# Kernel tuning notes

Measured on AMD Instinct MI355X. Metric: run time of the kernel, lower is better.

Reference implementation:

```python
import jax, jax.numpy as jnp
import numpy as np

BS, NE, IN_DIM = 1024, 128, 512
EMBED, OUT_DIM = 512, 512
N_HEADS, N_AGENTS = 8, 32
HEAD_DIM = EMBED // N_HEADS


def setup_inputs() -> dict:
    key = jax.random.key(0)
    ks = jax.random.split(key, 6)
    entities = jax.random.normal(ks[0], (BS, NE, IN_DIM), dtype=jnp.float32)
    pre_mask = jax.random.bernoulli(ks[1], 0.3, (BS, N_AGENTS, NE))
    post_mask = jax.random.bernoulli(ks[2], 0.3, (BS, N_AGENTS))
    # parameters (torch Linear convention: W @ x, i.e. [out, in])
    W_in = jax.random.normal(ks[3], (3 * EMBED, IN_DIM), dtype=jnp.float32) / np.sqrt(IN_DIM)
    W_out = jax.random.normal(ks[4], (OUT_DIM, EMBED), dtype=jnp.float32) / np.sqrt(EMBED)
    b_out = jax.random.normal(ks[5], (OUT_DIM,), dtype=jnp.float32) * 0.01
    return {"entities": entities, "pre_mask": pre_mask, "post_mask": post_mask,
            "W_in": W_in, "W_out": W_out, "b_out": b_out}


def reference(entities, pre_mask, post_mask, W_in, W_out, b_out):
    bs, ne, _ = entities.shape
    qkv = entities @ W_in.T                      # [bs, ne, 3*embed]
    q, k, v = jnp.split(qkv, 3, axis=-1)
    q = q[:, :N_AGENTS]                          # [bs, na, embed]
    q = q.reshape(bs, N_AGENTS, N_HEADS, HEAD_DIM)
    k = k.reshape(bs, ne, N_HEADS, HEAD_DIM)
    v = v.reshape(bs, ne, N_HEADS, HEAD_DIM)
    scale = jnp.sqrt(jnp.float32(HEAD_DIM))
    logits = jnp.einsum('bahd,behd->bhae', q, k) / scale   # [bs, h, na, ne]
    masked = jnp.where(pre_mask[:, None], -jnp.inf, logits)
    w = jax.nn.softmax(masked, axis=-1)
    w = jnp.where(jnp.isnan(w), 0.0, w)          # fully-masked rows -> 0 (NaN cleanup)
    attn = jnp.einsum('bhae,behd->bahd', w, v).reshape(bs, N_AGENTS, EMBED)
    out = attn @ W_out.T + b_out                 # [bs, na, out_dim]
    out = jnp.where(post_mask[:, :, None], 0.0, out)
    return out
```

## Files before the change

### kernel.cpp

```cpp
#include <hip/hip_runtime.h>
#include <hip/hip_bf16.h>
#include <stdint.h>


#define NE_ 128
#define NA_ 32
#define NH_ 8
#define HD_ 64
#define IND_ 512
#define EMB_ 512

typedef __attribute__((ext_vector_type(8))) __bf16 bf16x8;
typedef __attribute__((ext_vector_type(4))) float f32x4;

static __device__ __forceinline__ unsigned short bfu(float x) {
  __hip_bfloat16 h = __float2bfloat16(x);
  union { __hip_bfloat16 h1; unsigned short u; } c; c.h1 = h; return c.u;
}
static __device__ __forceinline__ unsigned int pack2(float x, float y) {
  return (unsigned int)bfu(x) | ((unsigned int)bfu(y) << 16);
}
static __device__ __forceinline__ void gload16(const void* g, const void* l) {
  __builtin_amdgcn_global_load_lds(
      (const __attribute__((address_space(1))) unsigned int*)g,
      (__attribute__((address_space(3))) unsigned int*)l, 16, 0, 0);
}

__global__ __launch_bounds__(256)
void k0_convert(const float* __restrict__ win, const float* __restrict__ wout,
                unsigned short* __restrict__ wb) {
  int t = blockIdx.x * 256 + threadIdx.x;
  int i = t * 4;
  float4 v;
  if (i < 786432) v = *(const float4*)(win + i);
  else            v = *(const float4*)(wout + (i - 786432));
  uint2 pk; pk.x = pack2(v.x, v.y); pk.y = pack2(v.z, v.w);
  *(uint2*)(wb + i) = pk;
}

struct K1Lds {
  union {
    struct { unsigned short a[128 * 64]; unsigned short b[192 * 64]; } st;
    struct {
      union { float s[32 * 132]; unsigned short attn[32 * 72]; } x;
      unsigned short p[32 * 136];
    } sm;
  } u;
  unsigned short kk[128 * 72];
  unsigned short vT[64 * 136];
  unsigned short qq[32 * 72];
};

__global__ __launch_bounds__(256, 2)
void k1_fused(const float* __restrict__ ent, const int* __restrict__ pre,
              const unsigned short* __restrict__ wb, unsigned short* __restrict__ attn_out) {
  __shared__ K1Lds sh;
  const int tid = threadIdx.x;
  const int w = tid >> 6, l = tid & 63;
  const int n = blockIdx.x;
  const int xcd = n & 7, kid = n >> 3;
  const int b = xcd * 128 + (kid >> 3);
  const int h = kid & 7;

  const float* E = ent + (size_t)b * (NE_ * IND_);
  char* aB = (char*)sh.u.st.a;
  char* bB = (char*)sh.u.st.b;

  f32x4 acc[2][12];
#pragma unroll
  for (int i = 0; i < 2; ++i)
#pragma unroll
    for (int j = 0; j < 12; ++j) acc[i][j] = (f32x4){0.f, 0.f, 0.f, 0.f};

  const int trow = tid >> 4, tc4 = tid & 15;
  const int hi16 = (l >> 4) << 4;

  for (int kt = 0; kt < 8; ++kt) {
    __syncthreads();
#pragma unroll
    for (int i = 0; i < 8; ++i) {
      int row = trow + i * 16;
      const float4 v = *(const float4*)(E + row * 512 + kt * 64 + tc4 * 4);
      uint2 pk; pk.x = pack2(v.x, v.y); pk.y = pack2(v.z, v.w);
      int x = (row * 128 + tc4 * 8) ^ ((row & 7) << 4);
      *(uint2*)(aB + x) = pk;
    }
#pragma unroll
    for (int i = 0; i < 6; ++i) {
      int c = w * 6 + i;
      int x = c * 1024 + l * 16;
      int y = x ^ (((x >> 7) & 7) << 4);
      int idx = y >> 1;
      int r = idx >> 6, col = idx & 63;
      int wrow = ((r >> 6) << 9) + h * 64 + (r & 63);
      gload16(wb + (size_t)wrow * 512 + kt * 64 + col, bB + c * 1024);
    }
    __syncthreads();
#pragma unroll
    for (int ks = 0; ks < 2; ++ks) {
      bf16x8 af[2];
#pragma unroll
      for (int i = 0; i < 2; ++i) {
        int row = (w * 2 + i) * 16 + (l & 15);
        int off = (row * 128 + ks * 64 + hi16) ^ ((row & 7) << 4);
        af[i] = *(const bf16x8*)(aB + off);
      }
#pragma unroll
      for (int j = 0; j < 12; ++j) {
        int r = j * 16 + (l & 15);
        int off = (r * 128 + ks * 64 + hi16) ^ ((r & 7) << 4);
        bf16x8 bf = *(const bf16x8*)(bB + off);
        acc[0][j] = __builtin_amdgcn_mfma_f32_16x16x32_bf16(af[0], bf, acc[0][j], 0, 0, 0);
        acc[1][j] = __builtin_amdgcn_mfma_f32_16x16x32_bf16(af[1], bf, acc[1][j], 0, 0, 0);
      }
    }
  }

  {
    const int col16 = l & 15, rg = l >> 4;
#pragma unroll
    for (int i = 0; i < 2; ++i) {
      int mrow = (w * 2 + i) * 16 + rg * 4;
      if (w == 0) {
#pragma unroll
        for (int j = 0; j < 4; ++j) {
          int d = j * 16 + col16;
#pragma unroll
          for (int r = 0; r < 4; ++r) sh.qq[(mrow + r) * 72 + d] = bfu(acc[i][j][r] * 0.125f);
        }
      }
#pragma unroll
      for (int j = 4; j < 8; ++j) {
        int d = (j - 4) * 16 + col16;
#pragma unroll
        for (int r = 0; r < 4; ++r) sh.kk[(mrow + r) * 72 + d] = bfu(acc[i][j][r]);
      }
#pragma unroll
      for (int j = 8; j < 12; ++j) {
        int d = (j - 8) * 16 + col16;
        uint2 pk;
        pk.x = pack2(acc[i][j][0], acc[i][j][1]);
        pk.y = pack2(acc[i][j][2], acc[i][j][3]);
        *(uint2*)((char*)sh.vT + d * 272 + mrow * 2) = pk;
      }
    }
  }
  __syncthreads();

  {
    f32x4 sacc[2][2];
#pragma unroll
    for (int i = 0; i < 2; ++i)
#pragma unroll
      for (int j = 0; j < 2; ++j) sacc[i][j] = (f32x4){0.f, 0.f, 0.f, 0.f};
    char* qB = (char*)sh.qq;
    char* kB = (char*)sh.kk;
#pragma unroll
    for (int ks = 0; ks < 2; ++ks) {
      bf16x8 qf[2];
#pragma unroll
      for (int at = 0; at < 2; ++at) {
        int row = at * 16 + (l & 15);
        qf[at] = *(const bf16x8*)(qB + row * 144 + ks * 64 + hi16);
      }
#pragma unroll
      for (int je = 0; je < 2; ++je) {
        int e = (2 * w + je) * 16 + (l & 15);
        bf16x8 kf = *(const bf16x8*)(kB + e * 144 + ks * 64 + hi16);
        sacc[0][je] = __builtin_amdgcn_mfma_f32_16x16x32_bf16(qf[0], kf, sacc[0][je], 0, 0, 0);
        sacc[1][je] = __builtin_amdgcn_mfma_f32_16x16x32_bf16(qf[1], kf, sacc[1][je], 0, 0, 0);
      }
    }
    float* S = sh.u.sm.x.s;
#pragma unroll
    for (int at = 0; at < 2; ++at)
#pragma unroll
      for (int je = 0; je < 2; ++je) {
        int e = (2 * w + je) * 16 + (l & 15);
        int a0 = at * 16 + (l >> 4) * 4;
#pragma unroll
        for (int r = 0; r < 4; ++r) S[(a0 + r) * 132 + e] = sacc[at][je][r];
      }
  }
  __syncthreads();

  {
    int a = tid >> 3, ls = tid & 7;
    const int* pm = pre + ((size_t)b * NA_ + a) * NE_ + ls * 16;
    const float* srow = sh.u.sm.x.s + a * 132 + ls * 16;
    float sv[16]; int mk[16];
    float mx = -__builtin_inff();
#pragma unroll
    for (int c = 0; c < 4; ++c) {
      int4 m4 = *(const int4*)(pm + c * 4);
      float4 s4 = *(const float4*)(srow + c * 4);
      mk[c * 4 + 0] = m4.x; sv[c * 4 + 0] = s4.x;
      mk[c * 4 + 1] = m4.y; sv[c * 4 + 1] = s4.y;
      mk[c * 4 + 2] = m4.z; sv[c * 4 + 2] = s4.z;
      mk[c * 4 + 3] = m4.w; sv[c * 4 + 3] = s4.w;
    }
#pragma unroll
    for (int i = 0; i < 16; ++i)
      if (!mk[i]) mx = fmaxf(mx, sv[i]);
    mx = fmaxf(mx, __shfl_xor(mx, 1));
    mx = fmaxf(mx, __shfl_xor(mx, 2));
    mx = fmaxf(mx, __shfl_xor(mx, 4));
    const bool dead = (mx == -__builtin_inff());
    float pv[16]; float sum = 0.f;
#pragma unroll
    for (int i = 0; i < 16; ++i) {
      float p = (mk[i] || dead) ? 0.f : __expf(sv[i] - mx);
      pv[i] = p; sum += p;
    }
    sum += __shfl_xor(sum, 1);
    sum += __shfl_xor(sum, 2);
    sum += __shfl_xor(sum, 4);
    float inv = dead ? 0.f : (1.f / sum);
    unsigned short* P = sh.u.sm.p + a * 136 + ls * 16;
#pragma unroll
    for (int c = 0; c < 4; ++c) {
      uint2 pk;
      pk.x = pack2(pv[c * 4 + 0] * inv, pv[c * 4 + 1] * inv);
      pk.y = pack2(pv[c * 4 + 2] * inv, pv[c * 4 + 3] * inv);
      *(uint2*)(P + c * 4) = pk;
    }
  }
  __syncthreads();

  {
    char* pB = (char*)sh.u.sm.p;
    char* vB = (char*)sh.vT;
    int at = w >> 1, dt0 = (w & 1) * 2;
    f32x4 pacc[2] = {(f32x4){0.f, 0.f, 0.f, 0.f}, (f32x4){0.f, 0.f, 0.f, 0.f}};
#pragma unroll
    for (int ks = 0; ks < 4; ++ks) {
      int arow = at * 16 + (l & 15);
      bf16x8 pf = *(const bf16x8*)(pB + arow * 272 + ks * 64 + hi16);
#pragma unroll
      for (int jd = 0; jd < 2; ++jd) {
        int d = (dt0 + jd) * 16 + (l & 15);
        bf16x8 vf = *(const bf16x8*)(vB + d * 272 + ks * 64 + hi16);
        pacc[jd] = __builtin_amdgcn_mfma_f32_16x16x32_bf16(pf, vf, pacc[jd], 0, 0, 0);
      }
    }
    unsigned short* A = sh.u.sm.x.attn;
#pragma unroll
    for (int jd = 0; jd < 2; ++jd) {
      int d = (dt0 + jd) * 16 + (l & 15);
      int a0 = at * 16 + (l >> 4) * 4;
#pragma unroll
      for (int r = 0; r < 4; ++r) A[(a0 + r) * 72 + d] = bfu(pacc[jd][r]);
    }
  }
  __syncthreads();

  {
    int row = tid >> 3, c8 = (tid & 7) * 8;
    uint4 v = *(const uint4*)((const char*)sh.u.sm.x.attn + row * 144 + c8 * 2);
    *(uint4*)(attn_out + ((size_t)(b * NA_ + row) * EMB_ + h * HD_ + c8)) = v;
  }
}

__global__ __launch_bounds__(256, 2)
void k2_out(const unsigned short* __restrict__ attn, const unsigned short* __restrict__ wob,
            const float* __restrict__ bout, const int* __restrict__ post,
            float* __restrict__ out) {
  __shared__ struct { unsigned short a[128 * 64]; unsigned short b[128 * 64]; } sh;
  const int tid = threadIdx.x, w = tid >> 6, l = tid & 63;
  const int n = blockIdx.x;
  const int sw = (n & 7) * 128 + (n >> 3);
  const int mt = sw >> 2, ntb = sw & 3;
  char* aB = (char*)sh.a;
  char* bB = (char*)sh.b;
  const int hi16 = (l >> 4) << 4;

  f32x4 acc[2][8];
#pragma unroll
  for (int i = 0; i < 2; ++i)
#pragma unroll
    for (int j = 0; j < 8; ++j) acc[i][j] = (f32x4){0.f, 0.f, 0.f, 0.f};

  for (int kt = 0; kt < 8; ++kt) {
    __syncthreads();
#pragma unroll
    for (int i = 0; i < 4; ++i) {
      int c = w * 4 + i;
      int x = c * 1024 + l * 16;
      int y = x ^ (((x >> 7) & 7) << 4);
      int idx = y >> 1, r = idx >> 6, col = idx & 63;
      gload16(attn + (size_t)(mt * 128 + r) * 512 + kt * 64 + col, aB + c * 1024);
      gload16(wob + (size_t)(ntb * 128 + r) * 512 + kt * 64 + col, bB + c * 1024);
    }
    __syncthreads();
#pragma unroll
    for (int ks = 0; ks < 2; ++ks) {
      bf16x8 af[2];
#pragma unroll
      for (int i = 0; i < 2; ++i) {
        int row = (w * 2 + i) * 16 + (l & 15);
        af[i] = *(const bf16x8*)(aB + ((row * 128 + ks * 64 + hi16) ^ ((row & 7) << 4)));
      }
#pragma unroll
      for (int j = 0; j < 8; ++j) {
        int r = j * 16 + (l & 15);
        bf16x8 bf = *(const bf16x8*)(bB + ((r * 128 + ks * 64 + hi16) ^ ((r & 7) << 4)));
        acc[0][j] = __builtin_amdgcn_mfma_f32_16x16x32_bf16(af[0], bf, acc[0][j], 0, 0, 0);
        acc[1][j] = __builtin_amdgcn_mfma_f32_16x16x32_bf16(af[1], bf, acc[1][j], 0, 0, 0);
      }
    }
  }

  int pmv[2][4];
#pragma unroll
  for (int i = 0; i < 2; ++i) {
    int m0 = mt * 128 + w * 32 + i * 16 + (l >> 4) * 4;
#pragma unroll
    for (int r = 0; r < 4; ++r) pmv[i][r] = post[m0 + r];
  }
#pragma unroll
  for (int j = 0; j < 8; ++j) {
    int nn = ntb * 128 + j * 16 + (l & 15);
    float bo = bout[nn];
#pragma unroll
    for (int i = 0; i < 2; ++i) {
      int m0 = mt * 128 + w * 32 + i * 16 + (l >> 4) * 4;
#pragma unroll
      for (int r = 0; r < 4; ++r) {
        float v = pmv[i][r] ? 0.f : (acc[i][j][r] + bo);
        out[(size_t)(m0 + r) * 512 + nn] = v;
      }
    }
  }
}

extern "C" void kernel_launch(void* const* d_in, const int* in_sizes, int n_in,
                              void* d_out, int out_size, void* d_ws, size_t ws_size,
                              hipStream_t stream) {
  const float* ent  = (const float*)d_in[0];
  const int*   pre  = (const int*)d_in[1];
  const int*   post = (const int*)d_in[2];
  const float* win  = (const float*)d_in[3];
  const float* wout = (const float*)d_in[4];
  const float* bout = (const float*)d_in[5];
  float* out = (float*)d_out;

  unsigned short* wsb   = (unsigned short*)d_ws;
  unsigned short* winb  = wsb;
  unsigned short* woutb = wsb + 786432;
  unsigned short* attnb = wsb + 1048576;

  hipLaunchKernelGGL(k0_convert, dim3(1024), dim3(256), 0, stream, win, wout, wsb);
  hipLaunchKernelGGL(k1_fused, dim3(8192), dim3(256), 0, stream, ent, pre, winb, attnb);
  hipLaunchKernelGGL(k2_out, dim3(1024), dim3(256), 0, stream, attnb, woutb, bout, post, out);
}
```

Measured before the change: 695.8 us.

## Split Q projection into own kernel, process two heads per block

Adds a separate GEMM kernel that projects only the 32 agent rows to Q and writes it to workspace. The fused attention kernel now covers two heads per 512-thread block and computes only K/V with larger 4x4 MFMA warp tiles. The old code computed Q for all 128 entities and discarded most of it. Fewer blocks each reread the entity tile and convert it to bf16, which cuts redundant fp32 reads and conversions. The output GEMM also moves to 256-row tiles with 512 threads. The cost is an extra launch, a Q round trip through global memory, and more LDS per block, which may limit occupancy.

```diff
diff --git a/kernel.cpp b/kernel.cpp
--- a/kernel.cpp
+++ b/kernel.cpp
@@ -2,13 +2,6 @@
 #include <hip/hip_bf16.h>
 #include <stdint.h>
 
-
-#define NE_ 128
-#define NA_ 32
-#define NH_ 8
-#define HD_ 64
-#define IND_ 512
-#define EMB_ 512
 
 typedef __attribute__((ext_vector_type(8))) __bf16 bf16x8;
 typedef __attribute__((ext_vector_type(4))) float f32x4;
@@ -38,295 +31,370 @@
   *(uint2*)(wb + i) = pk;
 }
 
+__global__ __launch_bounds__(256, 3)
+void kq_qproj(const float* __restrict__ ent, const unsigned short* __restrict__ wb,
+              unsigned short* __restrict__ q_ws) {
+  __shared__ union {
+    struct { unsigned short a[128 * 64]; unsigned short b[128 * 64]; } st;
+    unsigned short rs[128 * 136];
+  } sh;
+  const int tid = threadIdx.x, w = tid >> 6, l = tid & 63;
+  const int n = blockIdx.x;
+  const int sw = (n & 7) * 128 + (n >> 3);
+  const int mt = sw >> 2, ntb = sw & 3;
+  char* aB = (char*)sh.st.a;
+  char* bB = (char*)sh.st.b;
+  const int hi16 = (l >> 4) << 4;
+  const int trow = tid >> 4, tc4 = tid & 15;
+
+  f32x4 acc[2][8];
+#pragma unroll
+  for (int i = 0; i < 2; ++i)
+#pragma unroll
+    for (int j = 0; j < 8; ++j) acc[i][j] = (f32x4){0.f, 0.f, 0.f, 0.f};
+
+  for (int kt = 0; kt < 8; ++kt) {
+    __syncthreads();
+#pragma unroll
+    for (int i = 0; i < 8; ++i) {
+      int row = trow + i * 16;
+      int gr = mt * 128 + row;
+      const float4 v = *(const float4*)(ent + (size_t)(gr >> 5) * 65536 + (gr & 31) * 512 + kt * 64 + tc4 * 4);
+      uint2 pk; pk.x = pack2(v.x, v.y); pk.y = pack2(v.z, v.w);
+      int x = (row * 128 + tc4 * 8) ^ ((row & 7) << 4);
+      *(uint2*)(aB + x) = pk;
+    }
+#pragma unroll
+    for (int i = 0; i < 4; ++i) {
+      int c = w * 4 + i;
+      int x = c * 1024 + l * 16;
+      int y = x ^ (((x >> 7) & 7) << 4);
+      int idx = y >> 1, r = idx >> 6, col = idx & 63;
+      gload16(wb + (size_t)(ntb * 128 + r) * 512 + kt * 64 + col, bB + c * 1024);
+    }
+    __syncthreads();
+#pragma unroll
+    for (int ks = 0; ks < 2; ++ks) {
+      bf16x8 af[2];
+#pragma unroll
+      for (int i = 0; i < 2; ++i) {
+        int row = (w * 2 + i) * 16 + (l & 15);
+        af[i] = *(const bf16x8*)(aB + ((row * 128 + ks * 64 + hi16) ^ ((row & 7) << 4)));
+      }
+#pragma unroll
+      for (int j = 0; j < 8; ++j) {
+        int r = j * 16 + (l & 15);
+        bf16x8 bf = *(const bf16x8*)(bB + ((r * 128 + ks * 64 + hi16) ^ ((r & 7) << 4)));
+        acc[0][j] = __builtin_amdgcn_mfma_f32_16x16x32_bf16(af[0], bf, acc[0][j], 0, 0, 0);
+        acc[1][j] = __builtin_amdgcn_mfma_f32_16x16x32_bf16(af[1], bf, acc[1][j], 0, 0, 0);
+      }
+    }
+  }
+  __syncthreads();
+#pragma unroll
+  for (int i = 0; i < 2; ++i) {
+    int row0 = w * 32 + i * 16 + (l >> 4) * 4;
+#pragma unroll
+    for (int j = 0; j < 8; ++j) {
+      int col = j * 16 + (l & 15);
+#pragma unroll
+      for (int r = 0; r < 4; ++r) sh.rs[(row0 + r) * 136 + col] = bfu(acc[i][j][r] * 0.125f);
+    }
+  }
+  __syncthreads();
+#pragma unroll
+  for (int it = 0; it < 8; ++it) {
+    int row = it * 16 + (tid >> 4), c8 = (tid & 15) * 8;
+    uint4 v = *(const uint4*)((const char*)sh.rs + row * 272 + c8 * 2);
+    int gr = mt * 128 + row;
+    int b = gr >> 5, a = gr & 31;
+    int c = ntb * 128 + c8;
+    int h = c >> 6, d = c & 63;
+    *(uint4*)(q_ws + (((size_t)b * 8 + h) * 32 + a) * 64 + d) = v;
+  }
+}
+
 struct K1Lds {
   union {
-    struct { unsigned short a[128 * 64]; unsigned short b[192 * 64]; } st;
+    struct { unsigned short a[128 * 64]; unsigned short b[256 * 64]; } st;
     struct {
-      union { float s[32 * 132]; unsigned short attn[32 * 72]; } x;
+      unsigned short kk[128 * 72];
+      unsigned short vT[64 * 136];
+      unsigned short qq[32 * 72];
+      float s[32 * 132];
       unsigned short p[32 * 136];
+      unsigned short at[32 * 72];
     } sm;
   } u;
-  unsigned short kk[128 * 72];
-  unsigned short vT[64 * 136];
-  unsigned short qq[32 * 72];
 };
 
-__global__ __launch_bounds__(256, 2)
+__global__ __launch_bounds__(512, 4)
 void k1_fused(const float* __restrict__ ent, const int* __restrict__ pre,
-              const unsigned short* __restrict__ wb, unsigned short* __restrict__ attn_out) {
+              const unsigned short* __restrict__ wb, const unsigned short* __restrict__ q_ws,
+              unsigned short* __restrict__ attn_out) {
   __shared__ K1Lds sh;
   const int tid = threadIdx.x;
   const int w = tid >> 6, l = tid & 63;
   const int n = blockIdx.x;
   const int xcd = n & 7, kid = n >> 3;
-  const int b = xcd * 128 + (kid >> 3);
-  const int h = kid & 7;
-
-  const float* E = ent + (size_t)b * (NE_ * IND_);
+  const int b = xcd * 128 + (kid >> 2);
+  const int h2 = kid & 3;
+
+  const float* E = ent + (size_t)b * (128 * 512);
   char* aB = (char*)sh.u.st.a;
   char* bB = (char*)sh.u.st.b;
-
-  f32x4 acc[2][12];
-#pragma unroll
-  for (int i = 0; i < 2; ++i)
-#pragma unroll
-    for (int j = 0; j < 12; ++j) acc[i][j] = (f32x4){0.f, 0.f, 0.f, 0.f};
-
-  const int trow = tid >> 4, tc4 = tid & 15;
   const int hi16 = (l >> 4) << 4;
+  const int wr = w >> 2;
+  const int wq = w & 3;
+
+  f32x4 acc[4][4];
+#pragma unroll
+  for (int i = 0; i < 4; ++i)
+#pragma unroll
+    for (int j = 0; j < 4; ++j) acc[i][j] = (f32x4){0.f, 0.f, 0.f, 0.f};
 
   for (int kt = 0; kt < 8; ++kt) {
     __syncthreads();
-#pragma unroll
-    for (int i = 0; i < 8; ++i) {
-      int row = trow + i * 16;
-      const float4 v = *(const float4*)(E + row * 512 + kt * 64 + tc4 * 4);
-      uint2 pk; pk.x = pack2(v.x, v.y); pk.y = pack2(v.z, v.w);
-      int x = (row * 128 + tc4 * 8) ^ ((row & 7) << 4);
-      *(uint2*)(aB + x) = pk;
-    }
-#pragma unroll
-    for (int i = 0; i < 6; ++i) {
-      int c = w * 6 + i;
-      int x = c * 1024 + l * 16;
-      int y = x ^ (((x >> 7) & 7) << 4);
-      int idx = y >> 1;
-      int r = idx >> 6, col = idx & 63;
-      int wrow = ((r >> 6) << 9) + h * 64 + (r & 63);
-      gload16(wb + (size_t)wrow * 512 + kt * 64 + col, bB + c * 1024);
-    }
-    __syncthreads();
-#pragma unroll
-    for (int ks = 0; ks < 2; ++ks) {
-      bf16x8 af[2];
-#pragma unroll
-      for (int i = 0; i < 2; ++i) {
-        int row = (w * 2 + i) * 16 + (l & 15);
-        int off = (row * 128 + ks * 64 + hi16) ^ ((row & 7) << 4);
-        af[i] = *(const bf16x8*)(aB + off);
-      }
-#pragma unroll
-      for (int j = 0; j < 12; ++j) {
-        int r = j * 16 + (l & 15);
-        int off = (r * 128 + ks * 64 + hi16) ^ ((r & 7) << 4);
-        bf16x8 bf = *(const bf16x8*)(bB + off);
-        acc[0][j] = __builtin_amdgcn_mfma_f32_16x16x32_bf16(af[0], bf, acc[0][j], 0, 0, 0);
-        acc[1][j] = __builtin_amdgcn_mfma_f32_16x16x32_bf16(af[1], bf, acc[1][j], 0, 0, 0);
-      }
-    }
-  }
-
-  {
-    const int col16 = l & 15, rg = l >> 4;
-#pragma unroll
-    for (int i = 0; i < 2; ++i) {
-      int mrow = (w * 2 + i) * 16 + rg * 4;
-      if (w == 0) {
-#pragma unroll
-        for (int j = 0; j < 4; ++j) {
-          int d = j * 16 + col16;
-#pragma unroll
-          for (int r = 0; r < 4; ++r) sh.qq[(mrow + r) * 72 + d] = bfu(acc[i][j][r] * 0.125f);
-        }
-      }
-#pragma unroll
-      for (int j = 4; j < 8; ++j) {
-        int d = (j - 4) * 16 + col16;
-#pragma unroll
-        for (int r = 0; r < 4; ++r) sh.kk[(mrow + r) * 72 + d] = bfu(acc[i][j][r]);
-      }
-#pragma unroll
-      for (int j = 8; j < 12; ++j) {
-        int d = (j - 8) * 16 + col16;
-        uint2 pk;
-        pk.x = pack2(acc[i][j][0], acc[i][j][1]);
-        pk.y = pack2(acc[i][j][2], acc[i][j][3]);
-        *(uint2*)((char*)sh.vT + d * 272 + mrow * 2) = pk;
-      }
-    }
-  }
-  __syncthreads();
-
-  {
-    f32x4 sacc[2][2];
-#pragma unroll
-    for (int i = 0; i < 2; ++i)
-#pragma unroll
-      for (int j = 0; j < 2; ++j) sacc[i][j] = (f32x4){0.f, 0.f, 0.f, 0.f};
-    char* qB = (char*)sh.qq;
-    char* kB = (char*)sh.kk;
-#pragma unroll
-    for (int ks = 0; ks < 2; ++ks) {
-      bf16x8 qf[2];
-#pragma unroll
-      for (int at = 0; at < 2; ++at) {
-        int row = at * 16 + (l & 15);
-        qf[at] = *(const bf16x8*)(qB + row * 144 + ks * 64 + hi16);
-      }
-#pragma unroll
-      for (int je = 0; je < 2; ++je) {
-        int e = (2 * w + je) * 16 + (l & 15);
-        bf16x8 kf = *(const bf16x8*)(kB + e * 144 + ks * 64 + hi16);
-        sacc[0][je] = __builtin_amdgcn_mfma_f32_16x16x32_bf16(qf[0], kf, sacc[0][je], 0, 0, 0);
-        sacc[1][je] = __builtin_amdgcn_mfma_f32_16x16x32_bf16(qf[1], kf, sacc[1][je], 0, 0, 0);
-      }
-    }
-    float* S = sh.u.sm.x.s;
-#pragma unroll
-    for (int at = 0; at < 2; ++at)
-#pragma unroll
-      for (int je = 0; je < 2; ++je) {
-        int e = (2 * w + je) * 16 + (l & 15);
-        int a0 = at * 16 + (l >> 4) * 4;
-#pragma unroll
-        for (int r = 0; r < 4; ++r) S[(a0 + r) * 132 + e] = sacc[at][je][r];
-      }
-  }
-  __syncthreads();
-
-  {
-    int a = tid >> 3, ls = tid & 7;
-    const int* pm = pre + ((size_t)b * NA_ + a) * NE_ + ls * 16;
-    const float* srow = sh.u.sm.x.s + a * 132 + ls * 16;
-    float sv[16]; int mk[16];
-    float mx = -__builtin_inff();
-#pragma unroll
-    for (int c = 0; c < 4; ++c) {
-      int4 m4 = *(const int4*)(pm + c * 4);
-      float4 s4 = *(const float4*)(srow + c * 4);
-      mk[c * 4 + 0] = m4.x; sv[c * 4 + 0] = s4.x;
-      mk[c * 4 + 1] = m4.y; sv[c * 4 + 1] = s4.y;
-      mk[c * 4 + 2] = m4.z; sv[c * 4 + 2] = s4.z;
-      mk[c * 4 + 3] = m4.w; sv[c * 4 + 3] = s4.w;
-    }
-#pragma unroll
-    for (int i = 0; i < 16; ++i)
-      if (!mk[i]) mx = fmaxf(mx, sv[i]);
-    mx = fmaxf(mx, __shfl_xor(mx, 1));
-    mx = fmaxf(mx, __shfl_xor(mx, 2));
-    mx = fmaxf(mx, __shfl_xor(mx, 4));
-    const bool dead = (mx == -__builtin_inff());
-    float pv[16]; float sum = 0.f;
-#pragma unroll
-    for (int i = 0; i < 16; ++i) {
-      float p = (mk[i] || dead) ? 0.f : __expf(sv[i] - mx);
-      pv[i] = p; sum += p;
-    }
-    sum += __shfl_xor(sum, 1);
-    sum += __shfl_xor(sum, 2);
-    sum += __shfl_xor(sum, 4);
-    float inv = dead ? 0.f : (1.f / sum);
-    unsigned short* P = sh.u.sm.p + a * 136 + ls * 16;
-#pragma unroll
-    for (int c = 0; c < 4; ++c) {
-      uint2 pk;
-      pk.x = pack2(pv[c * 4 + 0] * inv, pv[c * 4 + 1] * inv);
-      pk.y = pack2(pv[c * 4 + 2] * inv, pv[c * 4 + 3] * inv);
-      *(uint2*)(P + c * 4) = pk;
-    }
-  }
-  __syncthreads();
-
-  {
-    char* pB = (char*)sh.u.sm.p;
-    char* vB = (char*)sh.vT;
-    int at = w >> 1, dt0 = (w & 1) * 2;
-    f32x4 pacc[2] = {(f32x4){0.f, 0.f, 0.f, 0.f}, (f32x4){0.f, 0.f, 0.f, 0.f}};
-#pragma unroll
-    for (int ks = 0; ks < 4; ++ks) {
-      int arow = at * 16 + (l & 15);
-      bf16x8 pf = *(const bf16x8*)(pB + arow * 272 + ks * 64 + hi16);
-#pragma unroll
-      for (int jd = 0; jd < 2; ++jd) {
-        int d = (dt0 + jd) * 16 + (l & 15);
-        bf16x8 vf = *(const bf16x8*)(vB + d * 272 + ks * 64 + hi16);
-        pacc[jd] = __builtin_amdgcn_mfma_f32_16x16x32_bf16(pf, vf, pacc[jd], 0, 0, 0);
-      }
-    }
-    unsigned short* A = sh.u.sm.x.attn;
-#pragma unroll
-    for (int jd = 0; jd < 2; ++jd) {
-      int d = (dt0 + jd) * 16 + (l & 15);
-      int a0 = at * 16 + (l >> 4) * 4;
-#pragma unroll
-      for (int r = 0; r < 4; ++r) A[(a0 + r) * 72 + d] = bfu(pacc[jd][r]);
-    }
-  }
-  __syncthreads();
-
-  {
-    int row = tid >> 3, c8 = (tid & 7) * 8;
-    uint4 v = *(const uint4*)((const char*)sh.u.sm.x.attn + row * 144 + c8 * 2);
-    *(uint4*)(attn_out + ((size_t)(b * NA_ + row) * EMB_ + h * HD_ + c8)) = v;
-  }
-}
-
-__global__ __launch_bounds__(256, 2)
-void k2_out(const unsigned short* __restrict__ attn, const unsigned short* __restrict__ wob,
-            const float* __restrict__ bout, const int* __restrict__ post,
-            float* __restrict__ out) {
-  __shared__ struct { unsigned short a[128 * 64]; unsigned short b[128 * 64]; } sh;
-  const int tid = threadIdx.x, w = tid >> 6, l = tid & 63;
-  const int n = blockIdx.x;
-  const int sw = (n & 7) * 128 + (n >> 3);
-  const int mt = sw >> 2, ntb = sw & 3;
-  char* aB = (char*)sh.a;
-  char* bB = (char*)sh.b;
-  const int hi16 = (l >> 4) << 4;
-
-  f32x4 acc[2][8];
-#pragma unroll
-  for (int i = 0; i < 2; ++i)
-#pragma unroll
-    for (int j = 0; j < 8; ++j) acc[i][j] = (f32x4){0.f, 0.f, 0.f, 0.f};
-
-  for (int kt = 0; kt < 8; ++kt) {
-    __syncthreads();
+    {
+      int col4 = tid & 15;
+#pragma unroll
+      for (int it = 0; it < 4; ++it) {
+        int row = (tid >> 4) + it * 32;
+        const float4 v = *(const float4*)(E + row * 512 + kt * 64 + col4 * 4);
+        uint2 pk; pk.x = pack2(v.x, v.y); pk.y = pack2(v.z, v.w);
+        int x = (row * 128 + col4 * 8) ^ ((row & 7) << 4);
+        *(uint2*)(aB + x) = pk;
+      }
+    }
 #pragma unroll
     for (int i = 0; i < 4; ++i) {
       int c = w * 4 + i;
       int x = c * 1024 + l * 16;
       int y = x ^ (((x >> 7) & 7) << 4);
       int idx = y >> 1, r = idx >> 6, col = idx & 63;
-      gload16(attn + (size_t)(mt * 128 + r) * 512 + kt * 64 + col, aB + c * 1024);
+      int wrow = 512 + ((r >> 6) & 1) * 512 + (h2 * 2 + (r >> 7)) * 64 + (r & 63);
+      gload16(wb + (size_t)wrow * 512 + kt * 64 + col, bB + c * 1024);
+    }
+    __syncthreads();
+#pragma unroll
+    for (int ks = 0; ks < 2; ++ks) {
+      bf16x8 af[4], bf[4];
+#pragma unroll
+      for (int i = 0; i < 4; ++i) {
+        int row = wr * 64 + i * 16 + (l & 15);
+        af[i] = *(const bf16x8*)(aB + ((row * 128 + ks * 64 + hi16) ^ ((row & 7) << 4)));
+      }
+#pragma unroll
+      for (int j = 0; j < 4; ++j) {
+        int r = (wq * 4 + j) * 16 + (l & 15);
+        bf[j] = *(const bf16x8*)(bB + ((r * 128 + ks * 64 + hi16) ^ ((r & 7) << 4)));
+      }
+#pragma unroll
+      for (int i = 0; i < 4; ++i)
+#pragma unroll
+        for (int j = 0; j < 4; ++j)
+          acc[i][j] = __builtin_amdgcn_mfma_f32_16x16x32_bf16(af[i], bf[j], acc[i][j], 0, 0, 0);
+    }
+  }
+  __syncthreads();
+
+  for (int h = 0; h < 2; ++h) {
+    if ((wq >> 1) == h) {
+      const int kv = wq & 1;
+#pragma unroll
+      for (int i = 0; i < 4; ++i) {
+        int e0 = wr * 64 + i * 16 + (l >> 4) * 4;
+#pragma unroll
+        for (int j = 0; j < 4; ++j) {
+          int d = j * 16 + (l & 15);
+          if (kv == 0) {
+#pragma unroll
+            for (int r = 0; r < 4; ++r) sh.u.sm.kk[(e0 + r) * 72 + d] = bfu(acc[i][j][r]);
+          } else {
+            uint2 pk;
+            pk.x = pack2(acc[i][j][0], acc[i][j][1]);
+            pk.y = pack2(acc[i][j][2], acc[i][j][3]);
+            *(uint2*)((char*)sh.u.sm.vT + d * 272 + e0 * 2) = pk;
+          }
+        }
+      }
+    }
+    if (tid < 256) {
+      int row = tid >> 3, c8 = (tid & 7) * 8;
+      uint4 v = *(const uint4*)(q_ws + (((size_t)b * 8 + h2 * 2 + h) * 32 + row) * 64 + c8);
+      *(uint4*)((char*)sh.u.sm.qq + row * 144 + c8 * 2) = v;
+    }
+    __syncthreads();
+
+    {
+      f32x4 sacc[2] = {(f32x4){0.f, 0.f, 0.f, 0.f}, (f32x4){0.f, 0.f, 0.f, 0.f}};
+      const int at = w >> 2;
+#pragma unroll
+      for (int ks = 0; ks < 2; ++ks) {
+        int arow = at * 16 + (l & 15);
+        bf16x8 qf = *(const bf16x8*)((char*)sh.u.sm.qq + arow * 144 + ks * 64 + hi16);
+#pragma unroll
+        for (int je = 0; je < 2; ++je) {
+          int e = ((w & 3) * 2 + je) * 16 + (l & 15);
+          bf16x8 kf = *(const bf16x8*)((char*)sh.u.sm.kk + e * 144 + ks * 64 + hi16);
+          sacc[je] = __builtin_amdgcn_mfma_f32_16x16x32_bf16(qf, kf, sacc[je], 0, 0, 0);
+        }
+      }
+#pragma unroll
+      for (int je = 0; je < 2; ++je) {
+        int e = ((w & 3) * 2 + je) * 16 + (l & 15);
+        int a0 = at * 16 + (l >> 4) * 4;
+#pragma unroll
+        for (int r = 0; r < 4; ++r) sh.u.sm.s[(a0 + r) * 132 + e] = sacc[je][r];
+      }
+    }
+    __syncthreads();
+
+    if (tid < 256) {
+      int a = tid >> 3, ls = tid & 7;
+      const int* pm = pre + ((size_t)b * 32 + a) * 128 + ls * 16;
+      const float* srow = sh.u.sm.s + a * 132 + ls * 16;
+      float sv[16]; int mk[16];
+      float mx = -__builtin_inff();
+#pragma unroll
+      for (int c = 0; c < 4; ++c) {
+        int4 m4 = *(const int4*)(pm + c * 4);
+        float4 s4 = *(const float4*)(srow + c * 4);
+        mk[c * 4 + 0] = m4.x; sv[c * 4 + 0] = s4.x;
+        mk[c * 4 + 1] = m4.y; sv[c * 4 + 1] = s4.y;
+        mk[c * 4 + 2] = m4.z; sv[c * 4 + 2] = s4.z;
+        mk[c * 4 + 3] = m4.w; sv[c * 4 + 3] = s4.w;
+      }
+#pragma unroll
+      for (int i = 0; i < 16; ++i)
+        if (!mk[i]) mx = fmaxf(mx, sv[i]);
+      mx = fmaxf(mx, __shfl_xor(mx, 1));
+      mx = fmaxf(mx, __shfl_xor(mx, 2));
+      mx = fmaxf(mx, __shfl_xor(mx, 4));
+      const bool dead = (mx == -__builtin_inff());
+      float pv[16]; float sum = 0.f;
+#pragma unroll
+      for (int i = 0; i < 16; ++i) {
+        float p = (mk[i] || dead) ? 0.f : __expf(sv[i] - mx);
+        pv[i] = p; sum += p;
+      }
+      sum += __shfl_xor(sum, 1);
+      sum += __shfl_xor(sum, 2);
+      sum += __shfl_xor(sum, 4);
+      float inv = dead ? 0.f : (1.f / sum);
+      unsigned short* P = sh.u.sm.p + a * 136 + ls * 16;
+#pragma unroll
+      for (int c = 0; c < 4; ++c) {
+        uint2 pk;
+        pk.x = pack2(pv[c * 4 + 0] * inv, pv[c * 4 + 1] * inv);
+        pk.y = pack2(pv[c * 4 + 2] * inv, pv[c * 4 + 3] * inv);
+        *(uint2*)(P + c * 4) = pk;
+      }
+    }
+    __syncthreads();
+
+    {
+      const int at = w >> 2, dt = w & 3;
+      f32x4 pacc = (f32x4){0.f, 0.f, 0.f, 0.f};
+#pragma unroll
+      for (int ks = 0; ks < 4; ++ks) {
+        int arow = at * 16 + (l & 15);
+        bf16x8 pf = *(const bf16x8*)((char*)sh.u.sm.p + arow * 272 + ks * 64 + hi16);
+        int d = dt * 16 + (l & 15);
+        bf16x8 vf = *(const bf16x8*)((char*)sh.u.sm.vT + d * 272 + ks * 64 + hi16);
+        pacc = __builtin_amdgcn_mfma_f32_16x16x32_bf16(pf, vf, pacc, 0, 0, 0);
+      }
+      int d = dt * 16 + (l & 15);
+      int a0 = at * 16 + (l >> 4) * 4;
+#pragma unroll
+      for (int r = 0; r < 4; ++r) sh.u.sm.at[(a0 + r) * 72 + d] = bfu(pacc[r]);
+    }
+    __syncthreads();
+
+    if (tid < 256) {
+      int row = tid >> 3, c8 = (tid & 7) * 8;
+      uint4 v = *(const uint4*)((const char*)sh.u.sm.at + row * 144 + c8 * 2);
+      *(uint4*)(attn_out + ((size_t)(b * 32 + row) * 512 + (h2 * 2 + h) * 64 + c8)) = v;
+    }
+    __syncthreads();
+  }
+}
+
+__global__ __launch_bounds__(512, 4)
+void k2_out(const unsigned short* __restrict__ attn, const unsigned short* __restrict__ wob,
+            const float* __restrict__ bout, const int* __restrict__ post,
+            float* __restrict__ out) {
+  __shared__ struct { unsigned short a[256 * 64]; unsigned short b[128 * 64]; } sh;
+  const int tid = threadIdx.x, w = tid >> 6, l = tid & 63;
+  const int n = blockIdx.x;
+  const int sw = (n & 7) * 64 + (n >> 3);
+  const int mt = sw >> 2, ntb = sw & 3;
+  const int wr = w >> 1, wc = w & 1;
+  char* aB = (char*)sh.a;
+  char* bB = (char*)sh.b;
+  const int hi16 = (l >> 4) << 4;
+
+  f32x4 acc[4][4];
+#pragma unroll
+  for (int i = 0; i < 4; ++i)
+#pragma unroll
+    for (int j = 0; j < 4; ++j) acc[i][j] = (f32x4){0.f, 0.f, 0.f, 0.f};
+
+  for (int kt = 0; kt < 8; ++kt) {
+    __syncthreads();
+#pragma unroll
+    for (int i = 0; i < 4; ++i) {
+      int c = w * 4 + i;
+      int x = c * 1024 + l * 16;
+      int y = x ^ (((x >> 7) & 7) << 4);
+      int idx = y >> 1, r = idx >> 6, col = idx & 63;
+      gload16(attn + (size_t)(mt * 256 + r) * 512 + kt * 64 + col, aB + c * 1024);
+    }
+#pragma unroll
+    for (int i = 0; i < 2; ++i) {
+      int c = w * 2 + i;
+      int x = c * 1024 + l * 16;
+      int y = x ^ (((x >> 7) & 7) << 4);
+      int idx = y >> 1, r = idx >> 6, col = idx & 63;
       gload16(wob + (size_t)(ntb * 128 + r) * 512 + kt * 64 + col, bB + c * 1024);
     }
     __syncthreads();
 #pragma unroll
     for (int ks = 0; ks < 2; ++ks) {
-      bf16x8 af[2];
-#pragma unroll
-      for (int i = 0; i < 2; ++i) {
-        int row = (w * 2 + i) * 16 + (l & 15);
+      bf16x8 af[4], bf[4];
+#pragma unroll
+      for (int i = 0; i < 4; ++i) {
+        int row = wr * 64 + i * 16 + (l & 15);
         af[i] = *(const bf16x8*)(aB + ((row * 128 + ks * 64 + hi16) ^ ((row & 7) << 4)));
       }
 #pragma unroll
-      for (int j = 0; j < 8; ++j) {
-        int r = j * 16 + (l & 15);
-        bf16x8 bf = *(const bf16x8*)(bB + ((r * 128 + ks * 64 + hi16) ^ ((r & 7) << 4)));
-        acc[0][j] = __builtin_amdgcn_mfma_f32_16x16x32_bf16(af[0], bf, acc[0][j], 0, 0, 0);
-        acc[1][j] = __builtin_amdgcn_mfma_f32_16x16x32_bf16(af[1], bf, acc[1][j], 0, 0, 0);
-      }
-    }
-  }
-
-  int pmv[2][4];
-#pragma unroll
-  for (int i = 0; i < 2; ++i) {
-    int m0 = mt * 128 + w * 32 + i * 16 + (l >> 4) * 4;
-#pragma unroll
-    for (int r = 0; r < 4; ++r) pmv[i][r] = post[m0 + r];
-  }
-#pragma unroll
-  for (int j = 0; j < 8; ++j) {
-    int nn = ntb * 128 + j * 16 + (l & 15);
-    float bo = bout[nn];
-#pragma unroll
-    for (int i = 0; i < 2; ++i) {
-      int m0 = mt * 128 + w * 32 + i * 16 + (l >> 4) * 4;
+      for (int j = 0; j < 4; ++j) {
+        int r = wc * 64 + j * 16 + (l & 15);
+        bf[j] = *(const bf16x8*)(bB + ((r * 128 + ks * 64 + hi16) ^ ((r & 7) << 4)));
+      }
+#pragma unroll
+      for (int i = 0; i < 4; ++i)
+#pragma unroll
+        for (int j = 0; j < 4; ++j)
+          acc[i][j] = __builtin_amdgcn_mfma_f32_16x16x32_bf16(af[i], bf[j], acc[i][j], 0, 0, 0);
+    }
+  }
+
+  float bo[4];
+#pragma unroll
+  for (int j = 0; j < 4; ++j) bo[j] = bout[ntb * 128 + wc * 64 + j * 16 + (l & 15)];
+#pragma unroll
+  for (int i = 0; i < 4; ++i) {
+    int m0 = mt * 256 + wr * 64 + i * 16 + (l >> 4) * 4;
+    int pmv[4];
+#pragma unroll
+    for (int r = 0; r < 4; ++r) pmv[r] = post[m0 + r];
+#pragma unroll
+    for (int j = 0; j < 4; ++j) {
+      int nn = ntb * 128 + wc * 64 + j * 16 + (l & 15);
 #pragma unroll
       for (int r = 0; r < 4; ++r) {
-        float v = pmv[i][r] ? 0.f : (acc[i][j][r] + bo);
+        float v = pmv[r] ? 0.f : (acc[i][j][r] + bo[j]);
         out[(size_t)(m0 + r) * 512 + nn] = v;
       }
     }
@@ -347,9 +415,11 @@
   unsigned short* wsb   = (unsigned short*)d_ws;
   unsigned short* winb  = wsb;
   unsigned short* woutb = wsb + 786432;
-  unsigned short* attnb = wsb + 1048576;
+  unsigned short* q_ws  = wsb + 1048576;
+  unsigned short* attnb = wsb + 17825792;
 
   hipLaunchKernelGGL(k0_convert, dim3(1024), dim3(256), 0, stream, win, wout, wsb);
-  hipLaunchKernelGGL(k1_fused, dim3(8192), dim3(256), 0, stream, ent, pre, winb, attnb);
-  hipLaunchKernelGGL(k2_out, dim3(1024), dim3(256), 0, stream, attnb, woutb, bout, post, out);
-}
+  hipLaunchKernelGGL(kq_qproj, dim3(1024), dim3(256), 0, stream, ent, winb, q_ws);
+  hipLaunchKernelGGL(k1_fused, dim3(4096), dim3(512), 0, stream, ent, pre, winb, q_ws, attnb);
+  hipLaunchKernelGGL(k2_out, dim3(512), dim3(512), 0, stream, attnb, woutb, bout, post, out);
+}
```

New measurement: 875.3 us. 1.26x slower.
